# Optimization experiments

Measured on AMD Instinct MI355X. Metric: run time of the kernel, lower is better.

Reference implementation:

```python
import jax, jax.numpy as jnp
import numpy as np

B = 2            # batch_size (number of windows)
W_SIZE = 2       # window_size
WIDTH = 256      # cart_pixel_width
TEMP = 0.01      # softmax_temp
EPS = 1e-12      # F.normalize eps


def _l2norm(x, axis):
    n = jnp.sqrt(jnp.sum(x * x, axis=axis, keepdims=True))
    return x / jnp.maximum(n, EPS)


def _bilinear(img, u, v):
    """align_corners=True bilinear sample. img: [C,H,W]; u,v: [N] pixel coords."""
    H, W = img.shape[-2], img.shape[-1]
    u0 = jnp.clip(jnp.floor(u), 0, W - 1)
    v0 = jnp.clip(jnp.floor(v), 0, H - 1)
    u1 = jnp.clip(u0 + 1, 0, W - 1)
    v1 = jnp.clip(v0 + 1, 0, H - 1)
    au = u - u0
    av = v - v0
    u0i, u1i = u0.astype(jnp.int32), u1.astype(jnp.int32)
    v0i, v1i = v0.astype(jnp.int32), v1.astype(jnp.int32)
    g = lambda vi, ui: img[:, vi, ui]  # [C,N]
    return (g(v0i, u0i) * (1 - au) * (1 - av) + g(v0i, u1i) * au * (1 - av)
            + g(v1i, u0i) * (1 - au) * av + g(v1i, u1i) * au * av)


def setup_inputs() -> dict:
    key = jax.random.key(0)
    k1, k2, k3, k4 = jax.random.split(key, 4)
    BW, C, N, S = B * W_SIZE, 248, 1024, 1
    return {
        "keypoint_scores": jax.random.normal(k1, (BW, S, N), dtype=jnp.float32),
        "keypoint_desc": jax.random.normal(k2, (BW, C, N), dtype=jnp.float32),
        "desc_dense": jax.random.normal(k3, (BW, C, WIDTH, WIDTH), dtype=jnp.float32),
        "times_img": jax.random.uniform(k4, (BW, 1, WIDTH, WIDTH), dtype=jnp.float32),
    }


def reference(keypoint_scores, keypoint_desc, desc_dense, times_img):
    BW, C, N = keypoint_desc.shape
    w = W_SIZE
    # frame index bookkeeping (same as the torch per-batch loop, vectorized)
    src_ids = jnp.arange(B) * w                                   # [B]
    tgt_ids = (jnp.arange(B)[:, None] * w
               + jnp.arange(1, w)[None, :]).reshape(-1)           # [B*(w-1)]

    # dense pixel coordinates [W^2, 2] in (u, v) order
    v, u = jnp.meshgrid(jnp.arange(WIDTH), jnp.arange(WIDTH), indexing='ij')
    coords = jnp.stack([u.reshape(-1), v.reshape(-1)], axis=1).astype(desc_dense.dtype)

    # normalized source dense descriptors [B, C, W^2]
    src = _l2norm(desc_dense[src_ids].reshape(B, C, -1), axis=1)
    # normalized target keypoint descriptors [B, w-1, C, N]
    tgt = _l2norm(keypoint_desc[tgt_ids].reshape(B, w - 1, C, N), axis=2)

    # dense correlation: [B, w-1, N, W^2]
    match_vals = jnp.einsum('bkcn,bcm->bknm', tgt, src)
    soft = jax.nn.softmax(match_vals / TEMP, axis=-1)
    # coordinate-weighted sum -> pseudo coords [B*(w-1), N, 2]
    pseudo_coords = jnp.einsum('bknm,md->bknd', soft, coords).reshape(B * (w - 1), N, 2)

    # bilinear-sample src times at pseudo coords (normalize->grid_sample round trip
    # with align_corners maps back to the same pixel coords; H == W here)
    src_times = jnp.repeat(times_img[src_ids], w - 1, axis=0)      # [B*(w-1),1,H,W]
    pseudo_times = jax.vmap(_bilinear)(src_times,
                                       pseudo_coords[..., 0],
                                       pseudo_coords[..., 1])      # [B*(w-1),1,N]

    return (pseudo_coords, keypoint_scores[tgt_ids], tgt_ids, pseudo_times)
```

## Files before the change

### kernel.cpp

```cpp
#include <hip/hip_runtime.h>
#include <math.h>

typedef int i32x4 __attribute__((ext_vector_type(4)));
typedef int i32x16 __attribute__((ext_vector_type(16)));

#define CC 248
#define MM 65536
#define NN 1024

__device__ __forceinline__ float fexp2(float x) { return __builtin_amdgcn_exp2f(x); }


__global__ __launch_bounds__(512)
void convB_kernel(const float* __restrict__ dense, char* __restrict__ Ag) {
    __shared__ char at[2][16][128][16];
    __shared__ float scr[4][128];
    const int bid = blockIdx.x;
    const int fb  = bid >> 9;
    const int p0  = (bid & 511) * 128;
    const int tid = threadIdx.x;
    const int row = tid & 127;
    const int q   = tid >> 7;

    const float* dptr = dense + (size_t)(2 * fb) * CC * MM + p0 + row;
    float v[64];
    float ss = 0.f;
#pragma unroll
    for (int i = 0; i < 64; ++i) {
        int c = q * 64 + i;
        float x = (c < CC) ? dptr[(size_t)c * MM] : 0.f;
        v[i] = x;
        ss += x * x;
    }
    scr[q][row] = ss;
    __syncthreads();
    float inv = 32768.0f / fmaxf(sqrtf(scr[0][row] + scr[1][row] + scr[2][row] + scr[3][row]), 1e-12f);

#pragma unroll
    for (int j = 0; j < 16; ++j) {
        unsigned w1 = 0, w0 = 0;
#pragma unroll
        for (int t = 0; t < 4; ++t) {
            float qv = fminf(fmaxf(rintf(v[j * 4 + t] * inv), -32768.f), 32639.f);
            int af = (int)qv;
            int a1 = (af + 128) >> 8;
            int a0 = af - (a1 << 8);
            w1 |= (unsigned)(a1 & 255) << (8 * t);
            w0 |= (unsigned)(a0 & 255) << (8 * t);
        }
        int c0 = q * 64 + j * 4;
        int kg = c0 >> 4, dw = (c0 >> 2) & 3;
        *(unsigned*)&at[0][kg][row][dw * 4] = w1;
        *(unsigned*)&at[1][kg][row][dw * 4] = w0;
    }
    __syncthreads();

    const int tile = p0 >> 8, rhalf = (p0 >> 7) & 1;
    char* outb = Ag + (size_t)(fb * 256 + tile) * 131072;
#pragma unroll
    for (int it = 0; it < 8; ++it) {
        int id = tid + it * 512;
        int pl = id >> 11, kg = (id >> 7) & 15, r2 = id & 127;
        i32x4 vv = *(const i32x4*)&at[pl][kg][r2][0];
        *(i32x4*)&outb[(size_t)pl * 65536 + kg * 4096 + (rhalf * 128 + r2) * 16] = vv;
    }
}

__global__ __launch_bounds__(256)
void convA_kernel(const float* __restrict__ kdesc, char* __restrict__ Bg) {
    __shared__ char bt[2][16][32][16];
    __shared__ float scr[8][32];
    const int bid = blockIdx.x;
    const int b   = bid >> 5;
    const int nt  = bid & 31;
    const int n0  = nt * 32;
    const int tid = threadIdx.x;
    const int col = tid & 31;
    const int q   = tid >> 5;

    const float* kp = kdesc + (size_t)(2 * b + 1) * CC * NN + n0 + col;
    float ss = 0.f;
    for (int i = 0; i < 31; ++i) {
        int c = q * 31 + i;
        float v = kp[(size_t)c * NN];
        ss += v * v;
    }
    scr[q][col] = ss;
    __syncthreads();
    float tot = 0.f;
#pragma unroll
    for (int k = 0; k < 8; ++k) tot += scr[k][col];
    float inv = 32768.0f / fmaxf(sqrtf(tot), 1e-12f);
    if (tid < 64) {
        int pl = tid >> 5, c2 = tid & 31;
        *(long*)&bt[pl][15][c2][8] = 0L;
    }
    __syncthreads();
    for (int i = 0; i < 31; ++i) {
        int c = q * 31 + i;
        float qq = fminf(fmaxf(rintf(kp[(size_t)c * NN] * inv), -32768.f), 32639.f);
        int af = (int)qq;
        int a1 = (af + 128) >> 8;
        int a0 = af - (a1 << 8);
        bt[0][c >> 4][col][c & 15] = (char)a1;
        bt[1][c >> 4][col][c & 15] = (char)a0;
    }
    __syncthreads();
    char* outb = Bg + (size_t)(b * 32 + nt) * 16384;
    const char* src = &bt[0][0][0][0];
#pragma unroll
    for (int it = 0; it < 4; ++it) {
        int id = tid + it * 256;
        *(i32x4*)&outb[(size_t)id * 16] = *(const i32x4*)&src[(size_t)id * 16];
    }
}

__global__ __launch_bounds__(256, 2)
void gemm_kernel(const char* __restrict__ Ag, const char* __restrict__ Bg,
                 float* __restrict__ partials) {
    __shared__ char lds[12288];

    const int bid  = blockIdx.x;
    const int xcd  = bid & 7;
    const int rest = bid >> 3;
    const int nchunk = rest & 3;
    const int pid  = xcd + 8 * (rest >> 2);
    const int b      = pid >> 6;
    const int mchunk = pid & 63;

    const int lane = threadIdx.x & 63;
    const int w    = threadIdx.x >> 6;
    const int lrow = lane & 31;
    const int lhi  = lane >> 5;

    const char* atile0 = Ag + ((size_t)b * 256 + mchunk * 4) * 131072;
    const char* bb     = Bg + (size_t)(b * 32 + nchunk * 8 + w * 2) * 16384;

    i32x4 bc[8][2][2];
#pragma unroll
    for (int kk = 0; kk < 8; ++kk)
#pragma unroll
        for (int pl = 0; pl < 2; ++pl)
#pragma unroll
            for (int bp = 0; bp < 2; ++bp)
                bc[kk][pl][bp] = *(const i32x4*)(bb + bp * 16384 + pl * 8192
                                                 + (kk * 2 + lhi) * 512 + lrow * 16);

    auto ISSUE = [&](int p, int slotOff) {
        const int mtn = p >> 2, kq = p & 3;
        const int tile = mtn >> 3, row0 = (mtn & 7) * 32;
        const char* src = atile0 + (size_t)tile * 131072 + (w >> 1) * 65536
                        + (kq * 4 + (w & 1) * 2 + lhi) * 4096 + (row0 + lrow) * 16;
        char* dst = &lds[slotOff + (w >> 1) * 2048 + (w & 1) * 1024];
        __builtin_amdgcn_global_load_lds(
            (const __attribute__((address_space(1))) void*)src,
            (__attribute__((address_space(3))) void*)dst, 16, 0, 0);
    };

    i32x16 accH[2], accX[2];
#pragma unroll
    for (int bp = 0; bp < 2; ++bp) { accH[bp] = (i32x16)(0); accX[bp] = (i32x16)(0); }
    float rm[2], rz[2], rsu[2], rsv[2];
#pragma unroll
    for (int bp = 0; bp < 2; ++bp) { rm[bp] = -INFINITY; rz[bp] = 0.f; rsu[bp] = 0.f; rsv[bp] = 0.f; }

    const float S2 = 100.0f * 1.4426950408889634f / 1073741824.0f;
    const float cH = 65536.0f * S2;
    const float cX = 256.0f * S2;

    ISSUE(0, 0);
    ISSUE(1, 4096);
    int slotR = 0, slotW = 8192;

    for (int mt = 0; mt < 32; ++mt) {
#pragma unroll
        for (int kq = 0; kq < 4; ++kq) {
            const int p = mt * 4 + kq;
            if (p < 127) asm volatile("s_waitcnt vmcnt(1)" ::: "memory");
            else         asm volatile("s_waitcnt vmcnt(0)" ::: "memory");
            asm volatile("s_barrier" ::: "memory");
            if (p + 2 < 128) ISSUE(p + 2, slotW);

#pragma unroll
            for (int j = 0; j < 2; ++j) {
                const int kk = kq * 2 + j;
                i32x4 a1 = *(const i32x4*)&lds[slotR + j * 1024 + lhi * 512 + lrow * 16];
                i32x4 a0 = *(const i32x4*)&lds[slotR + 2048 + j * 1024 + lhi * 512 + lrow * 16];
                __builtin_amdgcn_s_setprio(1);
#pragma unroll
                for (int bp = 0; bp < 2; ++bp) {
                    accH[bp] = __builtin_amdgcn_mfma_i32_32x32x32_i8(a1, bc[kk][0][bp], accH[bp], 0, 0, 0);
                    accX[bp] = __builtin_amdgcn_mfma_i32_32x32x32_i8(a1, bc[kk][1][bp], accX[bp], 0, 0, 0);
                    accX[bp] = __builtin_amdgcn_mfma_i32_32x32x32_i8(a0, bc[kk][0][bp], accX[bp], 0, 0, 0);
                }
                __builtin_amdgcn_s_setprio(0);
            }
            slotR = (slotR == 8192) ? 0 : slotR + 4096;
            slotW = (slotW == 8192) ? 0 : slotW + 4096;
        }

        const int mbase = mchunk * 1024 + mt * 32;
        const float ub = (float)((mbase & 255) + 4 * lhi);
        const float vcoord = (float)(mbase >> 8);
#pragma unroll
        for (int bp = 0; bp < 2; ++bp) {
            int hm = accH[bp][0];
#pragma unroll
            for (int r = 0; r < 16; ++r) {
                int h = accH[bp][r];
                hm = (h > hm) ? h : hm;
            }
            const float bx = (float)hm * cH;
            float tz = 0.f, tsur = 0.f;
#pragma unroll
            for (int r = 0; r < 16; ++r) {
                int dH = accH[bp][r] - hm;
                float e = fexp2(fmaf((float)dH, cH, (float)accX[bp][r] * cX));
                tz += e;
                tsur = fmaf(e, (float)((r & 3) + 8 * (r >> 2)), tsur);
            }
            float tsu = fmaf(ub, tz, tsur);
            float tsv = vcoord * tz;
            float nm = fmaxf(rm[bp], bx);
            float f1 = fexp2(rm[bp] - nm), f2 = fexp2(bx - nm);
            rz[bp]  = rz[bp]  * f1 + tz  * f2;
            rsu[bp] = rsu[bp] * f1 + tsu * f2;
            rsv[bp] = rsv[bp] * f1 + tsv * f2;
            rm[bp]  = nm;
            accH[bp] = (i32x16)(0); accX[bp] = (i32x16)(0);
        }
    }

#pragma unroll
    for (int bp = 0; bp < 2; ++bp) {
        float m2  = __shfl_xor(rm[bp], 32, 64);
        float z2  = __shfl_xor(rz[bp], 32, 64);
        float su2 = __shfl_xor(rsu[bp], 32, 64);
        float sv2 = __shfl_xor(rsv[bp], 32, 64);
        float nm = fmaxf(rm[bp], m2);
        float f1 = fexp2(rm[bp] - nm), f2 = fexp2(m2 - nm);
        rz[bp]  = rz[bp]  * f1 + z2  * f2;
        rsu[bp] = rsu[bp] * f1 + su2 * f2;
        rsv[bp] = rsv[bp] * f1 + sv2 * f2;
        rm[bp]  = nm;
    }
    if (lane < 32) {
#pragma unroll
        for (int bp = 0; bp < 2; ++bp) {
            int n = nchunk * 256 + w * 64 + bp * 32 + lrow;
            size_t idxp = ((size_t)b * NN + n) * 64 + mchunk;
            ((float4*)partials)[idxp] = make_float4(rm[bp], rz[bp], rsu[bp], rsv[bp]);
        }
    }
}

__global__ __launch_bounds__(256)
void combine_kernel(const float* __restrict__ partials,
                    const float* __restrict__ kscores,
                    const float* __restrict__ times,
                    float* __restrict__ out) {
    const int wg   = blockIdx.x * 4 + (threadIdx.x >> 6);
    const int lane = threadIdx.x & 63;
    const int b = wg >> 10, n = wg & 1023;
    const float4* pp = (const float4*)partials + (size_t)wg * 64;

    float4 p = pp[lane];
    float m = p.x, z = p.y, su = p.z, sv = p.w;
#pragma unroll
    for (int mask = 32; mask >= 1; mask >>= 1) {
        float m2  = __shfl_xor(m, mask, 64);
        float z2  = __shfl_xor(z, mask, 64);
        float su2 = __shfl_xor(su, mask, 64);
        float sv2 = __shfl_xor(sv, mask, 64);
        float nm = fmaxf(m, m2);
        float f1 = fexp2(m - nm), f2 = fexp2(m2 - nm);
        z = z * f1 + z2 * f2; su = su * f1 + su2 * f2; sv = sv * f1 + sv2 * f2; m = nm;
    }

    if (lane == 0) {
        float u = su / z, v = sv / z;
        out[(size_t)wg * 2 + 0] = u;
        out[(size_t)wg * 2 + 1] = v;
        out[4096 + wg] = kscores[(size_t)(2 * b + 1) * NN + n];
        if (wg == 0) { out[6144] = 1.0f; out[6145] = 3.0f; }

        const float* timg = times + (size_t)(2 * b) * MM;
        float u0 = fminf(fmaxf(floorf(u), 0.f), 255.f);
        float v0 = fminf(fmaxf(floorf(v), 0.f), 255.f);
        float u1 = fminf(u0 + 1.f, 255.f);
        float v1 = fminf(v0 + 1.f, 255.f);
        float au = u - u0, av = v - v0;
        int u0i = (int)u0, u1i = (int)u1, v0i = (int)v0, v1i = (int)v1;
        float t00 = timg[v0i * 256 + u0i], t01 = timg[v0i * 256 + u1i];
        float t10 = timg[v1i * 256 + u0i], t11 = timg[v1i * 256 + u1i];
        float t = t00 * (1.f - au) * (1.f - av) + t01 * au * (1.f - av)
                + t10 * (1.f - au) * av + t11 * au * av;
        out[6146 + wg] = t;
    }
}

extern "C" void kernel_launch(void* const* d_in, const int* in_sizes, int n_in,
                              void* d_out, int out_size, void* d_ws, size_t ws_size,
                              hipStream_t stream) {
    const float* kscores = (const float*)d_in[0];
    const float* kdesc   = (const float*)d_in[1];
    const float* dense   = (const float*)d_in[2];
    const float* times   = (const float*)d_in[3];
    float* out = (float*)d_out;

    char* Ag = (char*)d_ws;
    char* Bg = Ag + (size_t)2 * 256 * 131072;
    float* partials = (float*)(Bg + (size_t)2 * 32 * 16384);

    hipLaunchKernelGGL(convB_kernel,   dim3(1024), dim3(512), 0, stream, dense, Ag);
    hipLaunchKernelGGL(convA_kernel,   dim3(64),   dim3(256), 0, stream, kdesc, Bg);
    hipLaunchKernelGGL(gemm_kernel,    dim3(512),  dim3(256), 0, stream, Ag, Bg, partials);
    hipLaunchKernelGGL(combine_kernel, dim3(512),  dim3(256), 0, stream, partials, kscores, times, out);
}
```

Before: 149.2 us.

## Drop online softmax max via fixed exponent bound and overlap epilogue with MFMAs

The running max and rescaling are replaced by a constant offset (BASE=145). Because descriptors are L2-normalized, cosine is at most 1, so the scaled logit never exceeds about 144.3 in log2 units, and the offset keeps exp2 from overflowing. Partials now carry only z, su and sv, and the combine kernel becomes plain sums. The GEMM pipeline moves to larger stages (8 KB slots, two loads per issue) and runs the previous tile's exp epilogue interleaved with the next tile's MFMAs, aiming to hide epilogue latency. The trade-off is underflow: if the best similarity for a keypoint is low enough, every exp2 term can flush to zero.

```diff
diff --git a/kernel.cpp b/kernel.cpp
--- a/kernel.cpp
+++ b/kernel.cpp
@@ -118,7 +118,7 @@
 __global__ __launch_bounds__(256, 2)
 void gemm_kernel(const char* __restrict__ Ag, const char* __restrict__ Bg,
                  float* __restrict__ partials) {
-    __shared__ char lds[12288];
+    __shared__ char lds[24576];
 
     const int bid  = blockIdx.x;
     const int xcd  = bid & 7;
@@ -147,109 +147,119 @@
                                                  + (kk * 2 + lhi) * 512 + lrow * 16);
 
     auto ISSUE = [&](int p, int slotOff) {
-        const int mtn = p >> 2, kq = p & 3;
+        const int mtn = p >> 1, h = p & 1;
         const int tile = mtn >> 3, row0 = (mtn & 7) * 32;
-        const char* src = atile0 + (size_t)tile * 131072 + (w >> 1) * 65536
-                        + (kq * 4 + (w & 1) * 2 + lhi) * 4096 + (row0 + lrow) * 16;
-        char* dst = &lds[slotOff + (w >> 1) * 2048 + (w & 1) * 1024];
-        __builtin_amdgcn_global_load_lds(
-            (const __attribute__((address_space(1))) void*)src,
-            (__attribute__((address_space(3))) void*)dst, 16, 0, 0);
+#pragma unroll
+        for (int i = 0; i < 2; ++i) {
+            int c = w * 2 + i;
+            int pl = c >> 2, kkl = c & 3;
+            const char* src = atile0 + (size_t)tile * 131072 + pl * 65536
+                            + (h * 8 + kkl * 2 + lhi) * 4096 + (row0 + lrow) * 16;
+            char* dst = &lds[slotOff + pl * 4096 + kkl * 1024];
+            __builtin_amdgcn_global_load_lds(
+                (const __attribute__((address_space(1))) void*)src,
+                (__attribute__((address_space(3))) void*)dst, 16, 0, 0);
+        }
     };
 
     i32x16 accH[2], accX[2];
 #pragma unroll
     for (int bp = 0; bp < 2; ++bp) { accH[bp] = (i32x16)(0); accX[bp] = (i32x16)(0); }
-    float rm[2], rz[2], rsu[2], rsv[2];
-#pragma unroll
-    for (int bp = 0; bp < 2; ++bp) { rm[bp] = -INFINITY; rz[bp] = 0.f; rsu[bp] = 0.f; rsv[bp] = 0.f; }
+    float rz[2] = {0.f, 0.f}, rsu[2] = {0.f, 0.f}, rsv[2] = {0.f, 0.f};
 
     const float S2 = 100.0f * 1.4426950408889634f / 1073741824.0f;
     const float cH = 65536.0f * S2;
     const float cX = 256.0f * S2;
-
-    ISSUE(0, 0);
-    ISSUE(1, 4096);
-    int slotR = 0, slotW = 8192;
-
-    for (int mt = 0; mt < 32; ++mt) {
-#pragma unroll
-        for (int kq = 0; kq < 4; ++kq) {
-            const int p = mt * 4 + kq;
-            if (p < 127) asm volatile("s_waitcnt vmcnt(1)" ::: "memory");
-            else         asm volatile("s_waitcnt vmcnt(0)" ::: "memory");
-            asm volatile("s_barrier" ::: "memory");
-            if (p + 2 < 128) ISSUE(p + 2, slotW);
-
-#pragma unroll
-            for (int j = 0; j < 2; ++j) {
-                const int kk = kq * 2 + j;
-                i32x4 a1 = *(const i32x4*)&lds[slotR + j * 1024 + lhi * 512 + lrow * 16];
-                i32x4 a0 = *(const i32x4*)&lds[slotR + 2048 + j * 1024 + lhi * 512 + lrow * 16];
-                __builtin_amdgcn_s_setprio(1);
-#pragma unroll
-                for (int bp = 0; bp < 2; ++bp) {
-                    accH[bp] = __builtin_amdgcn_mfma_i32_32x32x32_i8(a1, bc[kk][0][bp], accH[bp], 0, 0, 0);
-                    accX[bp] = __builtin_amdgcn_mfma_i32_32x32x32_i8(a1, bc[kk][1][bp], accX[bp], 0, 0, 0);
-                    accX[bp] = __builtin_amdgcn_mfma_i32_32x32x32_i8(a0, bc[kk][0][bp], accX[bp], 0, 0, 0);
-                }
-                __builtin_amdgcn_s_setprio(0);
-            }
-            slotR = (slotR == 8192) ? 0 : slotR + 4096;
-            slotW = (slotW == 8192) ? 0 : slotW + 4096;
-        }
-
-        const int mbase = mchunk * 1024 + mt * 32;
+    const float BASE = 145.0f;
+
+    auto EPI = [&](int mtq) {
+        const int mbase = mchunk * 1024 + mtq * 32;
         const float ub = (float)((mbase & 255) + 4 * lhi);
         const float vcoord = (float)(mbase >> 8);
 #pragma unroll
         for (int bp = 0; bp < 2; ++bp) {
-            int hm = accH[bp][0];
+            float tz = 0.f, tsur = 0.f;
 #pragma unroll
             for (int r = 0; r < 16; ++r) {
-                int h = accH[bp][r];
-                hm = (h > hm) ? h : hm;
-            }
-            const float bx = (float)hm * cH;
-            float tz = 0.f, tsur = 0.f;
-#pragma unroll
-            for (int r = 0; r < 16; ++r) {
-                int dH = accH[bp][r] - hm;
-                float e = fexp2(fmaf((float)dH, cH, (float)accX[bp][r] * cX));
+                float e = fexp2(fmaf((float)accH[bp][r], cH,
+                                fmaf((float)accX[bp][r], cX, -BASE)));
                 tz += e;
                 tsur = fmaf(e, (float)((r & 3) + 8 * (r >> 2)), tsur);
             }
-            float tsu = fmaf(ub, tz, tsur);
-            float tsv = vcoord * tz;
-            float nm = fmaxf(rm[bp], bx);
-            float f1 = fexp2(rm[bp] - nm), f2 = fexp2(bx - nm);
-            rz[bp]  = rz[bp]  * f1 + tz  * f2;
-            rsu[bp] = rsu[bp] * f1 + tsu * f2;
-            rsv[bp] = rsv[bp] * f1 + tsv * f2;
-            rm[bp]  = nm;
+            rz[bp] += tz;
+            rsu[bp] += fmaf(ub, tz, tsur);
+            rsv[bp] = fmaf(vcoord, tz, rsv[bp]);
             accH[bp] = (i32x16)(0); accX[bp] = (i32x16)(0);
         }
-    }
+    };
+
+    ISSUE(0, 0);
+    ISSUE(1, 8192);
+    int slotR = 0, slotW = 16384;
+
+    for (int mt = 0; mt < 32; ++mt) {
+#pragma unroll
+        for (int h = 0; h < 2; ++h) {
+            const int p = mt * 2 + h;
+            if (p < 63) asm volatile("s_waitcnt vmcnt(2)" ::: "memory");
+            else        asm volatile("s_waitcnt vmcnt(0)" ::: "memory");
+            asm volatile("s_barrier" ::: "memory");
+            if (p + 2 < 64) ISSUE(p + 2, slotW);
+
+            i32x4 a1_0 = *(const i32x4*)&lds[slotR + 0 * 1024 + lhi * 512 + lrow * 16];
+            i32x4 a0_0 = *(const i32x4*)&lds[slotR + 4096 + 0 * 1024 + lhi * 512 + lrow * 16];
+            i32x4 a1_1 = *(const i32x4*)&lds[slotR + 1 * 1024 + lhi * 512 + lrow * 16];
+            i32x4 a0_1 = *(const i32x4*)&lds[slotR + 4096 + 1 * 1024 + lhi * 512 + lrow * 16];
+
+            if (h == 0 && mt > 0) EPI(mt - 1);
+
+            __builtin_amdgcn_s_setprio(1);
+#pragma unroll
+            for (int bp = 0; bp < 2; ++bp) {
+                accH[bp] = __builtin_amdgcn_mfma_i32_32x32x32_i8(a1_0, bc[h * 4 + 0][0][bp], accH[bp], 0, 0, 0);
+                accX[bp] = __builtin_amdgcn_mfma_i32_32x32x32_i8(a1_0, bc[h * 4 + 0][1][bp], accX[bp], 0, 0, 0);
+                accX[bp] = __builtin_amdgcn_mfma_i32_32x32x32_i8(a0_0, bc[h * 4 + 0][0][bp], accX[bp], 0, 0, 0);
+                accH[bp] = __builtin_amdgcn_mfma_i32_32x32x32_i8(a1_1, bc[h * 4 + 1][0][bp], accH[bp], 0, 0, 0);
+                accX[bp] = __builtin_amdgcn_mfma_i32_32x32x32_i8(a1_1, bc[h * 4 + 1][1][bp], accX[bp], 0, 0, 0);
+                accX[bp] = __builtin_amdgcn_mfma_i32_32x32x32_i8(a0_1, bc[h * 4 + 1][0][bp], accX[bp], 0, 0, 0);
+            }
+            __builtin_amdgcn_s_setprio(0);
+
+            i32x4 a1_2 = *(const i32x4*)&lds[slotR + 2 * 1024 + lhi * 512 + lrow * 16];
+            i32x4 a0_2 = *(const i32x4*)&lds[slotR + 4096 + 2 * 1024 + lhi * 512 + lrow * 16];
+            i32x4 a1_3 = *(const i32x4*)&lds[slotR + 3 * 1024 + lhi * 512 + lrow * 16];
+            i32x4 a0_3 = *(const i32x4*)&lds[slotR + 4096 + 3 * 1024 + lhi * 512 + lrow * 16];
+
+            __builtin_amdgcn_s_setprio(1);
+#pragma unroll
+            for (int bp = 0; bp < 2; ++bp) {
+                accH[bp] = __builtin_amdgcn_mfma_i32_32x32x32_i8(a1_2, bc[h * 4 + 2][0][bp], accH[bp], 0, 0, 0);
+                accX[bp] = __builtin_amdgcn_mfma_i32_32x32x32_i8(a1_2, bc[h * 4 + 2][1][bp], accX[bp], 0, 0, 0);
+                accX[bp] = __builtin_amdgcn_mfma_i32_32x32x32_i8(a0_2, bc[h * 4 + 2][0][bp], accX[bp], 0, 0, 0);
+                accH[bp] = __builtin_amdgcn_mfma_i32_32x32x32_i8(a1_3, bc[h * 4 + 3][0][bp], accH[bp], 0, 0, 0);
+                accX[bp] = __builtin_amdgcn_mfma_i32_32x32x32_i8(a1_3, bc[h * 4 + 3][1][bp], accX[bp], 0, 0, 0);
+                accX[bp] = __builtin_amdgcn_mfma_i32_32x32x32_i8(a0_3, bc[h * 4 + 3][0][bp], accX[bp], 0, 0, 0);
+            }
+            __builtin_amdgcn_s_setprio(0);
+
+            slotR = (slotR == 16384) ? 0 : slotR + 8192;
+            slotW = (slotW == 16384) ? 0 : slotW + 8192;
+        }
+    }
+    EPI(31);
 
 #pragma unroll
     for (int bp = 0; bp < 2; ++bp) {
-        float m2  = __shfl_xor(rm[bp], 32, 64);
-        float z2  = __shfl_xor(rz[bp], 32, 64);
-        float su2 = __shfl_xor(rsu[bp], 32, 64);
-        float sv2 = __shfl_xor(rsv[bp], 32, 64);
-        float nm = fmaxf(rm[bp], m2);
-        float f1 = fexp2(rm[bp] - nm), f2 = fexp2(m2 - nm);
-        rz[bp]  = rz[bp]  * f1 + z2  * f2;
-        rsu[bp] = rsu[bp] * f1 + su2 * f2;
-        rsv[bp] = rsv[bp] * f1 + sv2 * f2;
-        rm[bp]  = nm;
+        rz[bp]  += __shfl_xor(rz[bp],  32, 64);
+        rsu[bp] += __shfl_xor(rsu[bp], 32, 64);
+        rsv[bp] += __shfl_xor(rsv[bp], 32, 64);
     }
     if (lane < 32) {
 #pragma unroll
         for (int bp = 0; bp < 2; ++bp) {
             int n = nchunk * 256 + w * 64 + bp * 32 + lrow;
             size_t idxp = ((size_t)b * NN + n) * 64 + mchunk;
-            ((float4*)partials)[idxp] = make_float4(rm[bp], rz[bp], rsu[bp], rsv[bp]);
+            ((float4*)partials)[idxp] = make_float4(rz[bp], rsu[bp], rsv[bp], 0.f);
         }
     }
 }
@@ -265,16 +275,12 @@
     const float4* pp = (const float4*)partials + (size_t)wg * 64;
 
     float4 p = pp[lane];
-    float m = p.x, z = p.y, su = p.z, sv = p.w;
+    float z = p.x, su = p.y, sv = p.z;
 #pragma unroll
     for (int mask = 32; mask >= 1; mask >>= 1) {
-        float m2  = __shfl_xor(m, mask, 64);
-        float z2  = __shfl_xor(z, mask, 64);
-        float su2 = __shfl_xor(su, mask, 64);
-        float sv2 = __shfl_xor(sv, mask, 64);
-        float nm = fmaxf(m, m2);
-        float f1 = fexp2(m - nm), f2 = fexp2(m2 - nm);
-        z = z * f1 + z2 * f2; su = su * f1 + su2 * f2; sv = sv * f1 + sv2 * f2; m = nm;
+        z  += __shfl_xor(z,  mask, 64);
+        su += __shfl_xor(su, mask, 64);
+        sv += __shfl_xor(sv, mask, 64);
     }
 
     if (lane == 0) {
```

Result: faster. 136.7 us (-8.3%).
